# Kernel tuning notes

Measured on AMD Instinct MI355X. Metric: run time of the kernel, lower is better.

The kernel has to match this reference:

```python
import jax, jax.numpy as jnp
import numpy as np

B, G, K, KD = 16384, 17, 12, 16      # batch, games, kicks/game, kick feature dim
DK, DM, H, T = 16, 32, 2, 4          # d_kick, d_model, n_attn_heads, n_targets
SD, H1, H2, HH = 64, 256, 128, 32    # static_dim, backbone hidden dims, head hidden
AO = H * DM                          # attention output dim = 64
EPS = 1e-5
NEG_INF = float('-inf')


def setup_inputs() -> dict:
    ks = jax.random.split(jax.random.key(0), 18)
    n = lambda i, s, sc=0.05: jax.random.normal(ks[i], s, jnp.float32) * sc
    x_static = jax.random.normal(ks[0], (B, SD), jnp.float32)
    x_kicks = jax.random.normal(ks[1], (B, G, K, KD), jnp.float32)
    # masks: True = real game / kick; force position 0 valid so no row is fully padded
    outer_mask = jax.random.bernoulli(ks[2], 0.9, (B, G)).at[:, 0].set(True)
    inner_mask = jax.random.bernoulli(ks[3], 0.85, (B, G, K)).at[:, :, 0].set(True)
    return dict(
        x_static=x_static, x_kicks=x_kicks,
        W_ke=n(4, (KD, DK)), b_ke=jnp.zeros((DK,), jnp.float32),
        q_inner=n(5, (1, DK), 0.02),
        W_ge=n(6, (DK, DM)), b_ge=jnp.zeros((DM,), jnp.float32),
        pos_emb=n(7, (G, DM), 0.02),
        q_outer=n(8, (T * H, DM), 0.02),
        log_temp=jnp.zeros((T,), jnp.float32),
        ln_g=jnp.ones((T, AO), jnp.float32), ln_b=jnp.zeros((T, AO), jnp.float32),
        W1=n(9, (SD, H1)), b1=jnp.zeros((H1,), jnp.float32),
        g1=jnp.ones((H1,), jnp.float32), be1=jnp.zeros((H1,), jnp.float32),
        m1=n(10, (H1,)), v1=jax.random.uniform(ks[11], (H1,), jnp.float32) + 0.5,
        W2=n(12, (H1, H2)), b2=jnp.zeros((H2,), jnp.float32),
        g2=jnp.ones((H2,), jnp.float32), be2=jnp.zeros((H2,), jnp.float32),
        m2=n(13, (H2,)), v2=jax.random.uniform(ks[14], (H2,), jnp.float32) + 0.5,
        Wh1=n(15, (T, H2 + AO, HH)), bh1=jnp.zeros((T, HH), jnp.float32),
        Wh2=n(16, (T, HH)), bh2=jnp.zeros((T,), jnp.float32),
        outer_mask=outer_mask, inner_mask=inner_mask)


def _forward(x_static, x_kicks, W_ke, b_ke, q_inner, W_ge, b_ge, pos_emb,
             q_outer, log_temp, ln_g, ln_b, W1, b1, g1, be1, m1, v1,
             W2, b2, g2, be2, m2, v2, Wh1, bh1, Wh2, bh2,
             outer_mask, inner_mask):
    # kick encoder: Linear -> ReLU, [B,G,K,KD] -> [B,G,K,DK]
    kick_enc = jax.nn.relu(jnp.einsum('bgkd,de->bgke', x_kicks, W_ke) + b_ke)
    # inner AttentionPool: single learned query over kicks within each game
    ai = jnp.einsum('d,bgkd->bgk', q_inner[0], kick_enc) * (DK ** -0.5)
    ai = jnp.where(inner_mask, ai, NEG_INF)
    wi = jnp.nan_to_num(jax.nn.softmax(ai, axis=-1))       # all-masked rows -> 0
    per_game = jnp.einsum('bgk,bgkd->bgd', wi, kick_enc)   # [B,G,DK]
    # game encoder + learned positional embedding
    encoded = jax.nn.relu(per_game @ W_ge + b_ge) + pos_emb[None]  # [B,G,DM]
    # outer AttentionPool: T*H learned queries over games, per-target temperature
    ao = jnp.einsum('qd,bgd->bqg', q_outer, encoded) * (DM ** -0.5)
    ao = ao * jnp.repeat(jnp.exp(-log_temp), H)[None, :, None]
    ao = jnp.where(outer_mask[:, None, :], ao, NEG_INF)
    wo = jnp.nan_to_num(jax.nn.softmax(ao, axis=-1))
    pooled = jnp.einsum('bqg,bgd->bqd', wo, encoded).reshape(-1, T, AO)  # [B,T,64]
    # per-target LayerNorm on history vector
    mu = pooled.mean(-1, keepdims=True)
    var = ((pooled - mu) ** 2).mean(-1, keepdims=True)
    hist = (pooled - mu) * jax.lax.rsqrt(var + EPS) * ln_g[None] + ln_b[None]
    # backbone: Linear -> BatchNorm(eval) -> ReLU, x2 (dropout = identity in eval)
    z = jax.nn.relu((x_static @ W1 + b1 - m1) * jax.lax.rsqrt(v1 + EPS) * g1 + be1)
    z = jax.nn.relu((z @ W2 + b2 - m2) * jax.lax.rsqrt(v2 + EPS) * g2 + be2)
    # per-target heads on [shared_static ; history_vec]
    head_in = jnp.concatenate(
        [jnp.broadcast_to(z[:, None, :], (z.shape[0], T, H2)), hist], axis=-1)  # [B,T,192]
    h = jax.nn.relu(jnp.einsum('btd,tdh->bth', head_in, Wh1) + bh1[None])
    out = jnp.einsum('bth,th->bt', h, Wh2) + bh2[None]
    return jnp.maximum(out, 0.0)  # all targets non-negative (clamp, not softplus)


def reference(x_static, x_kicks, W_ke, b_ke, q_inner, W_ge, b_ge, pos_emb,
              q_outer, log_temp, ln_g, ln_b, W1, b1, g1, be1, m1, v1,
              W2, b2, g2, be2, m2, v2, Wh1, bh1, Wh2, bh2,
              outer_mask, inner_mask):
    return _forward(x_static, x_kicks, W_ke, b_ke, q_inner, W_ge, b_ge, pos_emb,
                    q_outer, log_temp, ln_g, ln_b, W1, b1, g1, be1, m1, v1,
                    W2, b2, g2, be2, m2, v2, Wh1, bh1, Wh2, bh2,
                    outer_mask, inner_mask)
```

## Files before the change

kernel.cpp:

```cpp
#include <hip/hip_runtime.h>
#include <math.h>

#define NEGM (-1e30f)

__device__ __forceinline__ float4 ld4(const float* p) { return *(const float4*)p; }
__device__ __forceinline__ void fma4(float4& a, float s, const float4 w) {
    a.x += s * w.x; a.y += s * w.y; a.z += s * w.z; a.w += s * w.w;
}
__device__ __forceinline__ float dot4(const float4 a, const float4 b) {
    return (a.x * b.x + a.y * b.y) + (a.z * b.z + a.w * b.w);
}
__device__ __forceinline__ void upd4(float4& p, float rm, float rw, const float4 a) {
    p.x = p.x * rm + rw * a.x; p.y = p.y * rm + rw * a.y;
    p.z = p.z * rm + rw * a.z; p.w = p.w * rm + rw * a.w;
}
__device__ __forceinline__ void relu4(float4& a) {
    a.x = fmaxf(a.x, 0.f); a.y = fmaxf(a.y, 0.f);
    a.z = fmaxf(a.z, 0.f); a.w = fmaxf(a.w, 0.f);
}

__global__ __launch_bounds__(256) void hist_kernel(
    const float* __restrict__ x_kicks,
    const float* __restrict__ W_ke, const float* __restrict__ b_ke,
    const float* __restrict__ q_inner,
    const float* __restrict__ W_ge, const float* __restrict__ b_ge,
    const float* __restrict__ pos_emb, const float* __restrict__ q_outer,
    const float* __restrict__ log_temp,
    const float* __restrict__ ln_g, const float* __restrict__ ln_b,
    const int* __restrict__ outer_mask, const int* __restrict__ inner_mask,
    float* __restrict__ hist)
{
    __shared__ float s_wge[512];
    __shared__ float s_qout[256];
    __shared__ float s_part[4][51 * 20];
    __shared__ float s_enc[4][17 * 36];
    __shared__ float s_ao[4][136];

    const int tid  = threadIdx.x;
    const int wid  = tid >> 6;
    const int lane = tid & 63;
    const int b    = blockIdx.x * 4 + wid;

    s_qout[tid] = q_outer[tid];
    s_wge[tid] = W_ge[tid];
    s_wge[tid + 256] = W_ge[tid + 256];
    __syncthreads();

    float* part = s_part[wid];
    float* enc  = s_enc[wid];
    float* ao   = s_ao[wid];

    {
        const int lp = (lane < 51) ? lane : 50;
        const float* xb = x_kicks + ((size_t)b * 204 + lp * 4) * 16;
        const int4 msk = *(const int4*)(inner_mask + (size_t)b * 204 + lp * 4);

        const float4 qi0 = ld4(q_inner + 0), qi1 = ld4(q_inner + 4);
        const float4 qi2 = ld4(q_inner + 8), qi3 = ld4(q_inner + 12);
        const float4 bk0 = ld4(b_ke + 0), bk1 = ld4(b_ke + 4);
        const float4 bk2 = ld4(b_ke + 8), bk3 = ld4(b_ke + 12);

        float m = NEGM, s = 0.f;
        float4 p0 = {0,0,0,0}, p1 = p0, p2 = p0, p3 = p0;

        #pragma unroll
        for (int pp = 0; pp < 4; ++pp) {
            float xs[16];
            {
                float4 x0 = ld4(xb + pp * 16 + 0), x1 = ld4(xb + pp * 16 + 4);
                float4 x2 = ld4(xb + pp * 16 + 8), x3 = ld4(xb + pp * 16 + 12);
                xs[0]=x0.x; xs[1]=x0.y; xs[2]=x0.z; xs[3]=x0.w;
                xs[4]=x1.x; xs[5]=x1.y; xs[6]=x1.z; xs[7]=x1.w;
                xs[8]=x2.x; xs[9]=x2.y; xs[10]=x2.z; xs[11]=x2.w;
                xs[12]=x3.x; xs[13]=x3.y; xs[14]=x3.z; xs[15]=x3.w;
            }
            float4 a0 = bk0, a1 = bk1, a2 = bk2, a3 = bk3;
            #pragma unroll
            for (int i = 0; i < 16; ++i) {
                float xi = xs[i];
                fma4(a0, xi, ld4(W_ke + i * 16 + 0));
                fma4(a1, xi, ld4(W_ke + i * 16 + 4));
                fma4(a2, xi, ld4(W_ke + i * 16 + 8));
                fma4(a3, xi, ld4(W_ke + i * 16 + 12));
            }
            relu4(a0); relu4(a1); relu4(a2); relu4(a3);

            float sc = (dot4(a0, qi0) + dot4(a1, qi1) + dot4(a2, qi2) + dot4(a3, qi3)) * 0.25f;
            int mk = (pp == 0) ? msk.x : (pp == 1) ? msk.y : (pp == 2) ? msk.z : msk.w;

            float scm = mk ? sc : NEGM;
            float mn = fmaxf(m, scm);
            float rm = __expf(m - mn);
            float rw = mk ? __expf(sc - mn) : 0.f;
            s = s * rm + rw;
            upd4(p0, rm, rw, a0); upd4(p1, rm, rw, a1);
            upd4(p2, rm, rw, a2); upd4(p3, rm, rw, a3);
            m = mn;
        }

        const int base = (lp / 3) * 3;
        float gm = fmaxf(fmaxf(__shfl(m, base), __shfl(m, base + 1)), __shfl(m, base + 2));
        float r  = __expf(m - gm);
        float sl = s * r;
        float gs = __shfl(sl, base) + __shfl(sl, base + 1) + __shfl(sl, base + 2);
        float c  = r / gs;
        p0.x*=c; p0.y*=c; p0.z*=c; p0.w*=c;
        p1.x*=c; p1.y*=c; p1.z*=c; p1.w*=c;
        p2.x*=c; p2.y*=c; p2.z*=c; p2.w*=c;
        p3.x*=c; p3.y*=c; p3.z*=c; p3.w*=c;
        if (lane < 51) {
            *(float4*)&part[lane * 20 + 0]  = p0;
            *(float4*)&part[lane * 20 + 4]  = p1;
            *(float4*)&part[lane * 20 + 8]  = p2;
            *(float4*)&part[lane * 20 + 12] = p3;
        }
    }
    __syncthreads();

    for (int t = lane; t < 136; t += 64) {
        const int g = t >> 3, dq = t & 7;
        const float* pp0 = &part[(3 * g) * 20];
        float4 acc = ld4(b_ge + dq * 4);
        #pragma unroll
        for (int i4 = 0; i4 < 4; ++i4) {
            float4 qa = *(float4*)(pp0 + i4 * 4);
            float4 qb = *(float4*)(pp0 + 20 + i4 * 4);
            float4 qc = *(float4*)(pp0 + 40 + i4 * 4);
            float4 pg4;
            pg4.x = qa.x + qb.x + qc.x; pg4.y = qa.y + qb.y + qc.y;
            pg4.z = qa.z + qb.z + qc.z; pg4.w = qa.w + qb.w + qc.w;
            fma4(acc, pg4.x, *(float4*)&s_wge[(i4 * 4 + 0) * 32 + dq * 4]);
            fma4(acc, pg4.y, *(float4*)&s_wge[(i4 * 4 + 1) * 32 + dq * 4]);
            fma4(acc, pg4.z, *(float4*)&s_wge[(i4 * 4 + 2) * 32 + dq * 4]);
            fma4(acc, pg4.w, *(float4*)&s_wge[(i4 * 4 + 3) * 32 + dq * 4]);
        }
        float4 pe = ld4(pos_emb + g * 32 + dq * 4);
        acc.x = fmaxf(acc.x, 0.f) + pe.x; acc.y = fmaxf(acc.y, 0.f) + pe.y;
        acc.z = fmaxf(acc.z, 0.f) + pe.z; acc.w = fmaxf(acc.w, 0.f) + pe.w;
        *(float4*)&enc[g * 36 + dq * 4] = acc;
    }
    __syncthreads();

    for (int t = lane; t < 136; t += 64) {
        const int q = t / 17, g = t - q * 17;
        float4 acc = {0.f, 0.f, 0.f, 0.f};
        #pragma unroll
        for (int i4 = 0; i4 < 8; ++i4) {
            float4 ev = *(float4*)&enc[g * 36 + i4 * 4];
            float4 qv = *(float4*)&s_qout[q * 32 + i4 * 4];
            acc.x += ev.x * qv.x; acc.y += ev.y * qv.y;
            acc.z += ev.z * qv.z; acc.w += ev.w * qv.w;
        }
        float sv = (acc.x + acc.y) + (acc.z + acc.w);
        sv *= 0.17677669529663687f * __expf(-log_temp[q >> 1]);
        ao[t] = outer_mask[b * 17 + g] ? sv : NEGM;
    }
    __syncthreads();

    {
        const int q = lane >> 3, j = lane & 7;
        float s0 = ao[q * 17 + j];
        float s1 = ao[q * 17 + j + 8];
        float s2 = (j == 0) ? ao[q * 17 + 16] : NEGM;
        float mx = fmaxf(fmaxf(s0, s1), s2);
        mx = fmaxf(mx, __shfl_xor(mx, 1));
        mx = fmaxf(mx, __shfl_xor(mx, 2));
        mx = fmaxf(mx, __shfl_xor(mx, 4));
        float e0 = __expf(s0 - mx), e1 = __expf(s1 - mx);
        float e2 = (j == 0) ? __expf(s2 - mx) : 0.f;
        float ssum = e0 + e1 + e2;
        ssum += __shfl_xor(ssum, 1);
        ssum += __shfl_xor(ssum, 2);
        ssum += __shfl_xor(ssum, 4);
        float inv = 1.f / ssum;
        ao[q * 17 + j] = e0 * inv;
        ao[q * 17 + j + 8] = e1 * inv;
        if (j == 0) ao[q * 17 + 16] = e2 * inv;
    }
    __syncthreads();

    {
        const int q = lane >> 3, dq = lane & 7;
        float4 acc = {0.f, 0.f, 0.f, 0.f};
        #pragma unroll
        for (int g = 0; g < 17; ++g) {
            float w = ao[q * 17 + g];
            fma4(acc, w, *(float4*)&enc[g * 36 + dq * 4]);
        }
        float sv = (acc.x + acc.y) + (acc.z + acc.w);
        sv += __shfl_xor(sv, 1); sv += __shfl_xor(sv, 2);
        sv += __shfl_xor(sv, 4); sv += __shfl_xor(sv, 8);
        float mu = sv * 0.015625f;
        float4 d;
        d.x = acc.x - mu; d.y = acc.y - mu; d.z = acc.z - mu; d.w = acc.w - mu;
        float v = (d.x * d.x + d.y * d.y) + (d.z * d.z + d.w * d.w);
        v += __shfl_xor(v, 1); v += __shfl_xor(v, 2);
        v += __shfl_xor(v, 4); v += __shfl_xor(v, 8);
        float rs = rsqrtf(v * 0.015625f + 1e-5f);
        float4 gam = ld4(ln_g + lane * 4);
        float4 bet = ld4(ln_b + lane * 4);
        float4 res;
        res.x = d.x * rs * gam.x + bet.x; res.y = d.y * rs * gam.y + bet.y;
        res.z = d.z * rs * gam.z + bet.z; res.w = d.w * rs * gam.w + bet.w;
        *(float4*)&hist[(size_t)b * 256 + lane * 4] = res;
    }
}

__global__ __launch_bounds__(256) void backbone_kernel(
    const float* __restrict__ x_static,
    const float* __restrict__ W1, const float* __restrict__ b1,
    const float* __restrict__ g1, const float* __restrict__ be1,
    const float* __restrict__ m1, const float* __restrict__ v1,
    const float* __restrict__ W2, const float* __restrict__ b2,
    const float* __restrict__ g2, const float* __restrict__ be2,
    const float* __restrict__ m2, const float* __restrict__ v2,
    const float* __restrict__ Wh1, const float* __restrict__ bh1,
    const float* __restrict__ Wh2, const float* __restrict__ bh2,
    const float* __restrict__ hist, float* __restrict__ out)
{
    __shared__ float s_x[16 * 64];
    __shared__ float s_z1[16 * 256];
    __shared__ float s_z2[16 * 132];

    const int tid = threadIdx.x;
    const int row0 = blockIdx.x * 16;

    *(float4*)&s_x[tid * 4] = ld4(x_static + (size_t)row0 * 64 + tid * 4);
    __syncthreads();

    {
        const int col = tid;
        float acc[16];
        #pragma unroll
        for (int r = 0; r < 16; ++r) acc[r] = 0.f;
        for (int k4 = 0; k4 < 16; ++k4) {
            float w0 = W1[(k4 * 4 + 0) * 256 + col];
            float w1 = W1[(k4 * 4 + 1) * 256 + col];
            float w2 = W1[(k4 * 4 + 2) * 256 + col];
            float w3 = W1[(k4 * 4 + 3) * 256 + col];
            #pragma unroll
            for (int r = 0; r < 16; ++r) {
                float4 xv = *(float4*)&s_x[r * 64 + k4 * 4];
                acc[r] += xv.x * w0 + xv.y * w1 + xv.z * w2 + xv.w * w3;
            }
        }
        float sc = rsqrtf(v1[col] + 1e-5f) * g1[col];
        float off = b1[col] - m1[col];
        float bb = be1[col];
        #pragma unroll
        for (int r = 0; r < 16; ++r)
            s_z1[r * 256 + col] = fmaxf((acc[r] + off) * sc + bb, 0.f);
    }
    __syncthreads();

    {
        const int col = tid & 127;
        const int r0 = (tid >> 7) * 8;
        float acc[8];
        #pragma unroll
        for (int r = 0; r < 8; ++r) acc[r] = 0.f;
        for (int k4 = 0; k4 < 64; ++k4) {
            float w0 = W2[(k4 * 4 + 0) * 128 + col];
            float w1 = W2[(k4 * 4 + 1) * 128 + col];
            float w2 = W2[(k4 * 4 + 2) * 128 + col];
            float w3 = W2[(k4 * 4 + 3) * 128 + col];
            #pragma unroll
            for (int r = 0; r < 8; ++r) {
                float4 zv = *(float4*)&s_z1[(r0 + r) * 256 + k4 * 4];
                acc[r] += zv.x * w0 + zv.y * w1 + zv.z * w2 + zv.w * w3;
            }
        }
        float sc = rsqrtf(v2[col] + 1e-5f) * g2[col];
        float off = b2[col] - m2[col];
        float bb = be2[col];
        #pragma unroll
        for (int r = 0; r < 8; ++r)
            s_z2[(r0 + r) * 132 + col] = fmaxf((acc[r] + off) * sc + bb, 0.f);
    }
    __syncthreads();

    {
        const int p = tid >> 2;
        const int gl = tid & 3;
        const int row = p >> 2;
        const int tgt = p & 3;
        const int j0 = gl * 8;

        float acc[8];
        #pragma unroll
        for (int j = 0; j < 8; ++j) acc[j] = bh1[tgt * 32 + j0 + j];

        const float* w1p = Wh1 + (size_t)tgt * 192 * 32 + j0;
        for (int d4 = 0; d4 < 32; ++d4) {
            float4 zv = *(float4*)&s_z2[row * 132 + d4 * 4];
            #pragma unroll
            for (int c = 0; c < 4; ++c) {
                float v = (c == 0) ? zv.x : (c == 1) ? zv.y : (c == 2) ? zv.z : zv.w;
                float4 a = ld4(w1p + (d4 * 4 + c) * 32);
                float4 bq = ld4(w1p + (d4 * 4 + c) * 32 + 4);
                acc[0] += v * a.x;  acc[1] += v * a.y;  acc[2] += v * a.z;  acc[3] += v * a.w;
                acc[4] += v * bq.x; acc[5] += v * bq.y; acc[6] += v * bq.z; acc[7] += v * bq.w;
            }
        }
        const float* hp = hist + (size_t)(row0 + row) * 256 + tgt * 64;
        const float* w1q = w1p + 128 * 32;
        for (int d4 = 0; d4 < 16; ++d4) {
            float4 hv = ld4(hp + d4 * 4);
            #pragma unroll
            for (int c = 0; c < 4; ++c) {
                float v = (c == 0) ? hv.x : (c == 1) ? hv.y : (c == 2) ? hv.z : hv.w;
                float4 a = ld4(w1q + (d4 * 4 + c) * 32);
                float4 bq = ld4(w1q + (d4 * 4 + c) * 32 + 4);
                acc[0] += v * a.x;  acc[1] += v * a.y;  acc[2] += v * a.z;  acc[3] += v * a.w;
                acc[4] += v * bq.x; acc[5] += v * bq.y; acc[6] += v * bq.z; acc[7] += v * bq.w;
            }
        }
        float ps = 0.f;
        #pragma unroll
        for (int j = 0; j < 8; ++j) ps += fmaxf(acc[j], 0.f) * Wh2[tgt * 32 + j0 + j];
        ps += __shfl_xor(ps, 1);
        ps += __shfl_xor(ps, 2);
        if (gl == 0) out[(size_t)(row0 + row) * 4 + tgt] = fmaxf(ps + bh2[tgt], 0.f);
    }
}

extern "C" void kernel_launch(void* const* d_in, const int* in_sizes, int n_in,
                              void* d_out, int out_size, void* d_ws, size_t ws_size,
                              hipStream_t stream) {
    const float* x_static = (const float*)d_in[0];
    const float* x_kicks  = (const float*)d_in[1];
    const float* W_ke     = (const float*)d_in[2];
    const float* b_ke     = (const float*)d_in[3];
    const float* q_inner  = (const float*)d_in[4];
    const float* W_ge     = (const float*)d_in[5];
    const float* b_ge     = (const float*)d_in[6];
    const float* pos_emb  = (const float*)d_in[7];
    const float* q_outer  = (const float*)d_in[8];
    const float* log_temp = (const float*)d_in[9];
    const float* ln_g     = (const float*)d_in[10];
    const float* ln_b     = (const float*)d_in[11];
    const float* W1       = (const float*)d_in[12];
    const float* b1       = (const float*)d_in[13];
    const float* g1       = (const float*)d_in[14];
    const float* be1      = (const float*)d_in[15];
    const float* m1       = (const float*)d_in[16];
    const float* v1       = (const float*)d_in[17];
    const float* W2       = (const float*)d_in[18];
    const float* b2       = (const float*)d_in[19];
    const float* g2       = (const float*)d_in[20];
    const float* be2      = (const float*)d_in[21];
    const float* m2       = (const float*)d_in[22];
    const float* v2       = (const float*)d_in[23];
    const float* Wh1      = (const float*)d_in[24];
    const float* bh1      = (const float*)d_in[25];
    const float* Wh2      = (const float*)d_in[26];
    const float* bh2      = (const float*)d_in[27];
    const int* outer_mask = (const int*)d_in[28];
    const int* inner_mask = (const int*)d_in[29];

    float* hist = (float*)d_ws;
    float* out  = (float*)d_out;

    hist_kernel<<<16384 / 4, 256, 0, stream>>>(
        x_kicks, W_ke, b_ke, q_inner, W_ge, b_ge, pos_emb, q_outer,
        log_temp, ln_g, ln_b, outer_mask, inner_mask, hist);

    backbone_kernel<<<16384 / 16, 256, 0, stream>>>(
        x_static, W1, b1, g1, be1, m1, v1, W2, b2, g2, be2, m2, v2,
        Wh1, bh1, Wh2, bh2, hist, out);
}
```

Before: 153.9 us.

## Use packed float2 FMA math and reorganize backbone GEMM thread mapping

Converts the kick encoder, backbone matmuls and head matmul to two-wide float vector types so the compiler can emit packed FP32 FMA instructions. W_ke is staged in shared memory. The per-game three-lane partial sums are now reduced with shuffles instead of through shared memory, which shrinks the shared buffer. The backbone layers are remapped so each thread computes two adjacent columns over fewer rows, which lowers redundant shared loads. This adds more shuffles and changes register pressure and the global weight access pattern.

```diff
diff --git a/kernel.cpp b/kernel.cpp
--- a/kernel.cpp
+++ b/kernel.cpp
@@ -2,21 +2,15 @@
 #include <math.h>
 
 #define NEGM (-1e30f)
+
+typedef float v2f __attribute__((ext_vector_type(2)));
 
 __device__ __forceinline__ float4 ld4(const float* p) { return *(const float4*)p; }
 __device__ __forceinline__ void fma4(float4& a, float s, const float4 w) {
     a.x += s * w.x; a.y += s * w.y; a.z += s * w.z; a.w += s * w.w;
 }
-__device__ __forceinline__ float dot4(const float4 a, const float4 b) {
-    return (a.x * b.x + a.y * b.y) + (a.z * b.z + a.w * b.w);
-}
-__device__ __forceinline__ void upd4(float4& p, float rm, float rw, const float4 a) {
-    p.x = p.x * rm + rw * a.x; p.y = p.y * rm + rw * a.y;
-    p.z = p.z * rm + rw * a.z; p.w = p.w * rm + rw * a.w;
-}
-__device__ __forceinline__ void relu4(float4& a) {
-    a.x = fmaxf(a.x, 0.f); a.y = fmaxf(a.y, 0.f);
-    a.z = fmaxf(a.z, 0.f); a.w = fmaxf(a.w, 0.f);
+__device__ __forceinline__ v2f max0v(v2f a) {
+    a.x = fmaxf(a.x, 0.f); a.y = fmaxf(a.y, 0.f); return a;
 }
 
 __global__ __launch_bounds__(256) void hist_kernel(
@@ -30,9 +24,10 @@
     const int* __restrict__ outer_mask, const int* __restrict__ inner_mask,
     float* __restrict__ hist)
 {
+    __shared__ float s_wke[256];
     __shared__ float s_wge[512];
     __shared__ float s_qout[256];
-    __shared__ float s_part[4][51 * 20];
+    __shared__ float s_pg[4][17 * 20];
     __shared__ float s_enc[4][17 * 36];
     __shared__ float s_ao[4][136];
 
@@ -41,27 +36,31 @@
     const int lane = tid & 63;
     const int b    = blockIdx.x * 4 + wid;
 
+    s_wke[tid] = W_ke[tid];
     s_qout[tid] = q_outer[tid];
     s_wge[tid] = W_ge[tid];
     s_wge[tid + 256] = W_ge[tid + 256];
     __syncthreads();
 
-    float* part = s_part[wid];
-    float* enc  = s_enc[wid];
-    float* ao   = s_ao[wid];
-
-    {
-        const int lp = (lane < 51) ? lane : 50;
-        const float* xb = x_kicks + ((size_t)b * 204 + lp * 4) * 16;
-        const int4 msk = *(const int4*)(inner_mask + (size_t)b * 204 + lp * 4);
-
-        const float4 qi0 = ld4(q_inner + 0), qi1 = ld4(q_inner + 4);
-        const float4 qi2 = ld4(q_inner + 8), qi3 = ld4(q_inner + 12);
-        const float4 bk0 = ld4(b_ke + 0), bk1 = ld4(b_ke + 4);
-        const float4 bk2 = ld4(b_ke + 8), bk3 = ld4(b_ke + 12);
+    float* pg  = s_pg[wid];
+    float* enc = s_enc[wid];
+    float* ao  = s_ao[wid];
+
+    if (lane < 51) {
+        const float* xb = x_kicks + ((size_t)b * 204 + lane * 4) * 16;
+        const int4 msk = *(const int4*)(inner_mask + (size_t)b * 204 + lane * 4);
+
+        v2f qv[8], bk[8];
+        #pragma unroll
+        for (int j = 0; j < 8; ++j) {
+            qv[j] = *(const v2f*)(q_inner + 2 * j);
+            bk[j] = *(const v2f*)(b_ke + 2 * j);
+        }
 
         float m = NEGM, s = 0.f;
-        float4 p0 = {0,0,0,0}, p1 = p0, p2 = p0, p3 = p0;
+        v2f p[8];
+        #pragma unroll
+        for (int j = 0; j < 8; ++j) p[j] = v2f{0.f, 0.f};
 
         #pragma unroll
         for (int pp = 0; pp < 4; ++pp) {
@@ -74,18 +73,23 @@
                 xs[8]=x2.x; xs[9]=x2.y; xs[10]=x2.z; xs[11]=x2.w;
                 xs[12]=x3.x; xs[13]=x3.y; xs[14]=x3.z; xs[15]=x3.w;
             }
-            float4 a0 = bk0, a1 = bk1, a2 = bk2, a3 = bk3;
+            v2f a[8];
+            #pragma unroll
+            for (int j = 0; j < 8; ++j) a[j] = bk[j];
             #pragma unroll
             for (int i = 0; i < 16; ++i) {
-                float xi = xs[i];
-                fma4(a0, xi, ld4(W_ke + i * 16 + 0));
-                fma4(a1, xi, ld4(W_ke + i * 16 + 4));
-                fma4(a2, xi, ld4(W_ke + i * 16 + 8));
-                fma4(a3, xi, ld4(W_ke + i * 16 + 12));
-            }
-            relu4(a0); relu4(a1); relu4(a2); relu4(a3);
-
-            float sc = (dot4(a0, qi0) + dot4(a1, qi1) + dot4(a2, qi2) + dot4(a3, qi3)) * 0.25f;
+                v2f xi = {xs[i], xs[i]};
+                const v2f* wrow = (const v2f*)&s_wke[i * 16];
+                #pragma unroll
+                for (int j = 0; j < 8; ++j) a[j] += xi * wrow[j];
+            }
+            #pragma unroll
+            for (int j = 0; j < 8; ++j) a[j] = max0v(a[j]);
+
+            v2f dv = {0.f, 0.f};
+            #pragma unroll
+            for (int j = 0; j < 8; ++j) dv += a[j] * qv[j];
+            float sc = (dv.x + dv.y) * 0.25f;
             int mk = (pp == 0) ? msk.x : (pp == 1) ? msk.y : (pp == 2) ? msk.z : msk.w;
 
             float scm = mk ? sc : NEGM;
@@ -93,46 +97,45 @@
             float rm = __expf(m - mn);
             float rw = mk ? __expf(sc - mn) : 0.f;
             s = s * rm + rw;
-            upd4(p0, rm, rw, a0); upd4(p1, rm, rw, a1);
-            upd4(p2, rm, rw, a2); upd4(p3, rm, rw, a3);
+            v2f rmv = {rm, rm}, rwv = {rw, rw};
+            #pragma unroll
+            for (int j = 0; j < 8; ++j) p[j] = p[j] * rmv + a[j] * rwv;
             m = mn;
         }
 
-        const int base = (lp / 3) * 3;
+        const int base = (lane / 3) * 3;
         float gm = fmaxf(fmaxf(__shfl(m, base), __shfl(m, base + 1)), __shfl(m, base + 2));
         float r  = __expf(m - gm);
         float sl = s * r;
         float gs = __shfl(sl, base) + __shfl(sl, base + 1) + __shfl(sl, base + 2);
         float c  = r / gs;
-        p0.x*=c; p0.y*=c; p0.z*=c; p0.w*=c;
-        p1.x*=c; p1.y*=c; p1.z*=c; p1.w*=c;
-        p2.x*=c; p2.y*=c; p2.z*=c; p2.w*=c;
-        p3.x*=c; p3.y*=c; p3.z*=c; p3.w*=c;
-        if (lane < 51) {
-            *(float4*)&part[lane * 20 + 0]  = p0;
-            *(float4*)&part[lane * 20 + 4]  = p1;
-            *(float4*)&part[lane * 20 + 8]  = p2;
-            *(float4*)&part[lane * 20 + 12] = p3;
+        v2f cv = {c, c};
+        #pragma unroll
+        for (int j = 0; j < 8; ++j) p[j] *= cv;
+
+        float o[16];
+        #pragma unroll
+        for (int j = 0; j < 8; ++j) {
+            o[2*j]   = __shfl(p[j].x, base) + __shfl(p[j].x, base + 1) + __shfl(p[j].x, base + 2);
+            o[2*j+1] = __shfl(p[j].y, base) + __shfl(p[j].y, base + 1) + __shfl(p[j].y, base + 2);
+        }
+        if (lane == base) {
+            const int g = lane / 3;
+            *(float4*)&pg[g * 20 + 0]  = make_float4(o[0],  o[1],  o[2],  o[3]);
+            *(float4*)&pg[g * 20 + 4]  = make_float4(o[4],  o[5],  o[6],  o[7]);
+            *(float4*)&pg[g * 20 + 8]  = make_float4(o[8],  o[9],  o[10], o[11]);
+            *(float4*)&pg[g * 20 + 12] = make_float4(o[12], o[13], o[14], o[15]);
         }
     }
     __syncthreads();
 
     for (int t = lane; t < 136; t += 64) {
         const int g = t >> 3, dq = t & 7;
-        const float* pp0 = &part[(3 * g) * 20];
         float4 acc = ld4(b_ge + dq * 4);
         #pragma unroll
-        for (int i4 = 0; i4 < 4; ++i4) {
-            float4 qa = *(float4*)(pp0 + i4 * 4);
-            float4 qb = *(float4*)(pp0 + 20 + i4 * 4);
-            float4 qc = *(float4*)(pp0 + 40 + i4 * 4);
-            float4 pg4;
-            pg4.x = qa.x + qb.x + qc.x; pg4.y = qa.y + qb.y + qc.y;
-            pg4.z = qa.z + qb.z + qc.z; pg4.w = qa.w + qb.w + qc.w;
-            fma4(acc, pg4.x, *(float4*)&s_wge[(i4 * 4 + 0) * 32 + dq * 4]);
-            fma4(acc, pg4.y, *(float4*)&s_wge[(i4 * 4 + 1) * 32 + dq * 4]);
-            fma4(acc, pg4.z, *(float4*)&s_wge[(i4 * 4 + 2) * 32 + dq * 4]);
-            fma4(acc, pg4.w, *(float4*)&s_wge[(i4 * 4 + 3) * 32 + dq * 4]);
+        for (int i = 0; i < 16; ++i) {
+            float pv = pg[g * 20 + i];
+            fma4(acc, pv, *(float4*)&s_wge[i * 32 + dq * 4]);
         }
         float4 pe = ld4(pos_emb + g * 32 + dq * 4);
         acc.x = fmaxf(acc.x, 0.f) + pe.x; acc.y = fmaxf(acc.y, 0.f) + pe.y;
@@ -147,9 +150,9 @@
         #pragma unroll
         for (int i4 = 0; i4 < 8; ++i4) {
             float4 ev = *(float4*)&enc[g * 36 + i4 * 4];
-            float4 qv = *(float4*)&s_qout[q * 32 + i4 * 4];
-            acc.x += ev.x * qv.x; acc.y += ev.y * qv.y;
-            acc.z += ev.z * qv.z; acc.w += ev.w * qv.w;
+            float4 qvv = *(float4*)&s_qout[q * 32 + i4 * 4];
+            acc.x += ev.x * qvv.x; acc.y += ev.y * qvv.y;
+            acc.z += ev.z * qvv.z; acc.w += ev.w * qvv.w;
         }
         float sv = (acc.x + acc.y) + (acc.z + acc.w);
         sv *= 0.17677669529663687f * __expf(-log_temp[q >> 1]);
@@ -229,53 +232,70 @@
     __syncthreads();
 
     {
-        const int col = tid;
-        float acc[16];
-        #pragma unroll
-        for (int r = 0; r < 16; ++r) acc[r] = 0.f;
+        const int cp = tid & 127;
+        const int r0 = (tid >> 7) * 8;
+        v2f acc[8];
+        #pragma unroll
+        for (int r = 0; r < 8; ++r) acc[r] = v2f{0.f, 0.f};
         for (int k4 = 0; k4 < 16; ++k4) {
-            float w0 = W1[(k4 * 4 + 0) * 256 + col];
-            float w1 = W1[(k4 * 4 + 1) * 256 + col];
-            float w2 = W1[(k4 * 4 + 2) * 256 + col];
-            float w3 = W1[(k4 * 4 + 3) * 256 + col];
-            #pragma unroll
-            for (int r = 0; r < 16; ++r) {
-                float4 xv = *(float4*)&s_x[r * 64 + k4 * 4];
-                acc[r] += xv.x * w0 + xv.y * w1 + xv.z * w2 + xv.w * w3;
-            }
-        }
-        float sc = rsqrtf(v1[col] + 1e-5f) * g1[col];
-        float off = b1[col] - m1[col];
-        float bb = be1[col];
-        #pragma unroll
-        for (int r = 0; r < 16; ++r)
-            s_z1[r * 256 + col] = fmaxf((acc[r] + off) * sc + bb, 0.f);
-    }
-    __syncthreads();
-
-    {
-        const int col = tid & 127;
-        const int r0 = (tid >> 7) * 8;
-        float acc[8];
-        #pragma unroll
-        for (int r = 0; r < 8; ++r) acc[r] = 0.f;
+            float4 xv[8];
+            #pragma unroll
+            for (int r = 0; r < 8; ++r) xv[r] = *(float4*)&s_x[(r0 + r) * 64 + k4 * 4];
+            #pragma unroll
+            for (int c = 0; c < 4; ++c) {
+                v2f w2 = *(const v2f*)&W1[(k4 * 4 + c) * 256 + 2 * cp];
+                #pragma unroll
+                for (int r = 0; r < 8; ++r) {
+                    float xc = (c == 0) ? xv[r].x : (c == 1) ? xv[r].y : (c == 2) ? xv[r].z : xv[r].w;
+                    v2f xb = {xc, xc};
+                    acc[r] += xb * w2;
+                }
+            }
+        }
+        v2f v1v = *(const v2f*)(v1 + 2 * cp);
+        v2f g1v = *(const v2f*)(g1 + 2 * cp);
+        v2f b1v = *(const v2f*)(b1 + 2 * cp);
+        v2f m1v = *(const v2f*)(m1 + 2 * cp);
+        v2f e1v = *(const v2f*)(be1 + 2 * cp);
+        v2f scv; scv.x = rsqrtf(v1v.x + 1e-5f) * g1v.x; scv.y = rsqrtf(v1v.y + 1e-5f) * g1v.y;
+        v2f offv = b1v - m1v;
+        #pragma unroll
+        for (int r = 0; r < 8; ++r)
+            *(v2f*)&s_z1[(r0 + r) * 256 + 2 * cp] = max0v((acc[r] + offv) * scv + e1v);
+    }
+    __syncthreads();
+
+    {
+        const int cp = tid & 63;
+        const int q = tid >> 6;
+        v2f acc[4];
+        #pragma unroll
+        for (int r = 0; r < 4; ++r) acc[r] = v2f{0.f, 0.f};
         for (int k4 = 0; k4 < 64; ++k4) {
-            float w0 = W2[(k4 * 4 + 0) * 128 + col];
-            float w1 = W2[(k4 * 4 + 1) * 128 + col];
-            float w2 = W2[(k4 * 4 + 2) * 128 + col];
-            float w3 = W2[(k4 * 4 + 3) * 128 + col];
-            #pragma unroll
-            for (int r = 0; r < 8; ++r) {
-                float4 zv = *(float4*)&s_z1[(r0 + r) * 256 + k4 * 4];
-                acc[r] += zv.x * w0 + zv.y * w1 + zv.z * w2 + zv.w * w3;
-            }
-        }
-        float sc = rsqrtf(v2[col] + 1e-5f) * g2[col];
-        float off = b2[col] - m2[col];
-        float bb = be2[col];
-        #pragma unroll
-        for (int r = 0; r < 8; ++r)
-            s_z2[(r0 + r) * 132 + col] = fmaxf((acc[r] + off) * sc + bb, 0.f);
+            float4 zv[4];
+            #pragma unroll
+            for (int r = 0; r < 4; ++r) zv[r] = *(float4*)&s_z1[(4 * q + r) * 256 + k4 * 4];
+            #pragma unroll
+            for (int c = 0; c < 4; ++c) {
+                v2f w2 = *(const v2f*)&W2[(k4 * 4 + c) * 128 + 2 * cp];
+                #pragma unroll
+                for (int r = 0; r < 4; ++r) {
+                    float zc = (c == 0) ? zv[r].x : (c == 1) ? zv[r].y : (c == 2) ? zv[r].z : zv[r].w;
+                    v2f zb = {zc, zc};
+                    acc[r] += zb * w2;
+                }
+            }
+        }
+        v2f v2v = *(const v2f*)(v2 + 2 * cp);
+        v2f g2v = *(const v2f*)(g2 + 2 * cp);
+        v2f b2v = *(const v2f*)(b2 + 2 * cp);
+        v2f m2v = *(const v2f*)(m2 + 2 * cp);
+        v2f e2v = *(const v2f*)(be2 + 2 * cp);
+        v2f scv; scv.x = rsqrtf(v2v.x + 1e-5f) * g2v.x; scv.y = rsqrtf(v2v.y + 1e-5f) * g2v.y;
+        v2f offv = b2v - m2v;
+        #pragma unroll
+        for (int r = 0; r < 4; ++r)
+            *(v2f*)&s_z2[(4 * q + r) * 132 + 2 * cp] = max0v((acc[r] + offv) * scv + e2v);
     }
     __syncthreads();
 
@@ -286,9 +306,9 @@
         const int tgt = p & 3;
         const int j0 = gl * 8;
 
-        float acc[8];
-        #pragma unroll
-        for (int j = 0; j < 8; ++j) acc[j] = bh1[tgt * 32 + j0 + j];
+        v2f acc[4];
+        #pragma unroll
+        for (int j = 0; j < 4; ++j) acc[j] = *(const v2f*)(bh1 + tgt * 32 + j0 + 2 * j);
 
         const float* w1p = Wh1 + (size_t)tgt * 192 * 32 + j0;
         for (int d4 = 0; d4 < 32; ++d4) {
@@ -296,10 +316,10 @@
             #pragma unroll
             for (int c = 0; c < 4; ++c) {
                 float v = (c == 0) ? zv.x : (c == 1) ? zv.y : (c == 2) ? zv.z : zv.w;
-                float4 a = ld4(w1p + (d4 * 4 + c) * 32);
-                float4 bq = ld4(w1p + (d4 * 4 + c) * 32 + 4);
-                acc[0] += v * a.x;  acc[1] += v * a.y;  acc[2] += v * a.z;  acc[3] += v * a.w;
-                acc[4] += v * bq.x; acc[5] += v * bq.y; acc[6] += v * bq.z; acc[7] += v * bq.w;
+                v2f vb = {v, v};
+                const v2f* wp = (const v2f*)(w1p + (d4 * 4 + c) * 32);
+                #pragma unroll
+                for (int j = 0; j < 4; ++j) acc[j] += vb * wp[j];
             }
         }
         const float* hp = hist + (size_t)(row0 + row) * 256 + tgt * 64;
@@ -309,15 +329,18 @@
             #pragma unroll
             for (int c = 0; c < 4; ++c) {
                 float v = (c == 0) ? hv.x : (c == 1) ? hv.y : (c == 2) ? hv.z : hv.w;
-                float4 a = ld4(w1q + (d4 * 4 + c) * 32);
-                float4 bq = ld4(w1q + (d4 * 4 + c) * 32 + 4);
-                acc[0] += v * a.x;  acc[1] += v * a.y;  acc[2] += v * a.z;  acc[3] += v * a.w;
-                acc[4] += v * bq.x; acc[5] += v * bq.y; acc[6] += v * bq.z; acc[7] += v * bq.w;
+                v2f vb = {v, v};
+                const v2f* wp = (const v2f*)(w1q + (d4 * 4 + c) * 32);
+                #pragma unroll
+                for (int j = 0; j < 4; ++j) acc[j] += vb * wp[j];
             }
         }
         float ps = 0.f;
         #pragma unroll
-        for (int j = 0; j < 8; ++j) ps += fmaxf(acc[j], 0.f) * Wh2[tgt * 32 + j0 + j];
+        for (int j = 0; j < 4; ++j) {
+            ps += fmaxf(acc[j].x, 0.f) * Wh2[tgt * 32 + j0 + 2 * j];
+            ps += fmaxf(acc[j].y, 0.f) * Wh2[tgt * 32 + j0 + 2 * j + 1];
+        }
         ps += __shfl_xor(ps, 1);
         ps += __shfl_xor(ps, 2);
         if (gl == 0) out[(size_t)(row0 + row) * 4 + tgt] = fmaxf(ps + bh2[tgt], 0.f);
```

After: 161.2 us. +4.7%, slower.

## Stage W_ke in LDS, reduce game partials via shuffles, halve hist block size

Applied to the files above, without the earlier changes.

Moves the kick-encoder weight matrix into shared memory so the inner FMA loop reads LDS instead of global/constant loads. The three per-lane partial pooled vectors for each game are now summed with wavefront shuffles and written once per game, which shrinks the shared partial buffer and simplifies the W_ge projection loop. The hist kernel now runs 2 waves (128 threads) per block instead of 4, which lowers LDS use per block and allows more blocks per CU. The costs are extra shuffle instructions and more, smaller blocks.

```diff
diff --git a/kernel.cpp b/kernel.cpp
--- a/kernel.cpp
+++ b/kernel.cpp
@@ -14,12 +14,8 @@
     p.x = p.x * rm + rw * a.x; p.y = p.y * rm + rw * a.y;
     p.z = p.z * rm + rw * a.z; p.w = p.w * rm + rw * a.w;
 }
-__device__ __forceinline__ void relu4(float4& a) {
-    a.x = fmaxf(a.x, 0.f); a.y = fmaxf(a.y, 0.f);
-    a.z = fmaxf(a.z, 0.f); a.w = fmaxf(a.w, 0.f);
-}
-
-__global__ __launch_bounds__(256) void hist_kernel(
+
+__global__ __launch_bounds__(128) void hist_kernel(
     const float* __restrict__ x_kicks,
     const float* __restrict__ W_ke, const float* __restrict__ b_ke,
     const float* __restrict__ q_inner,
@@ -30,30 +26,35 @@
     const int* __restrict__ outer_mask, const int* __restrict__ inner_mask,
     float* __restrict__ hist)
 {
+    __shared__ float s_wke[256];
     __shared__ float s_wge[512];
     __shared__ float s_qout[256];
-    __shared__ float s_part[4][51 * 20];
-    __shared__ float s_enc[4][17 * 36];
-    __shared__ float s_ao[4][136];
+    __shared__ float s_pg[2][17 * 20];
+    __shared__ float s_enc[2][17 * 36];
+    __shared__ float s_ao[2][136];
 
     const int tid  = threadIdx.x;
     const int wid  = tid >> 6;
     const int lane = tid & 63;
-    const int b    = blockIdx.x * 4 + wid;
-
+    const int b    = blockIdx.x * 2 + wid;
+
+    s_wke[tid] = W_ke[tid];
+    s_wke[tid + 128] = W_ke[tid + 128];
     s_qout[tid] = q_outer[tid];
+    s_qout[tid + 128] = q_outer[tid + 128];
     s_wge[tid] = W_ge[tid];
+    s_wge[tid + 128] = W_ge[tid + 128];
     s_wge[tid + 256] = W_ge[tid + 256];
-    __syncthreads();
-
-    float* part = s_part[wid];
-    float* enc  = s_enc[wid];
-    float* ao   = s_ao[wid];
-
-    {
-        const int lp = (lane < 51) ? lane : 50;
-        const float* xb = x_kicks + ((size_t)b * 204 + lp * 4) * 16;
-        const int4 msk = *(const int4*)(inner_mask + (size_t)b * 204 + lp * 4);
+    s_wge[tid + 384] = W_ge[tid + 384];
+    __syncthreads();
+
+    float* pg  = s_pg[wid];
+    float* enc = s_enc[wid];
+    float* ao  = s_ao[wid];
+
+    if (lane < 51) {
+        const float* xb = x_kicks + ((size_t)b * 204 + lane * 4) * 16;
+        const int4 msk = *(const int4*)(inner_mask + (size_t)b * 204 + lane * 4);
 
         const float4 qi0 = ld4(q_inner + 0), qi1 = ld4(q_inner + 4);
         const float4 qi2 = ld4(q_inner + 8), qi3 = ld4(q_inner + 12);
@@ -78,12 +79,15 @@
             #pragma unroll
             for (int i = 0; i < 16; ++i) {
                 float xi = xs[i];
-                fma4(a0, xi, ld4(W_ke + i * 16 + 0));
-                fma4(a1, xi, ld4(W_ke + i * 16 + 4));
-                fma4(a2, xi, ld4(W_ke + i * 16 + 8));
-                fma4(a3, xi, ld4(W_ke + i * 16 + 12));
-            }
-            relu4(a0); relu4(a1); relu4(a2); relu4(a3);
+                fma4(a0, xi, *(float4*)&s_wke[i * 16 + 0]);
+                fma4(a1, xi, *(float4*)&s_wke[i * 16 + 4]);
+                fma4(a2, xi, *(float4*)&s_wke[i * 16 + 8]);
+                fma4(a3, xi, *(float4*)&s_wke[i * 16 + 12]);
+            }
+            a0.x=fmaxf(a0.x,0.f); a0.y=fmaxf(a0.y,0.f); a0.z=fmaxf(a0.z,0.f); a0.w=fmaxf(a0.w,0.f);
+            a1.x=fmaxf(a1.x,0.f); a1.y=fmaxf(a1.y,0.f); a1.z=fmaxf(a1.z,0.f); a1.w=fmaxf(a1.w,0.f);
+            a2.x=fmaxf(a2.x,0.f); a2.y=fmaxf(a2.y,0.f); a2.z=fmaxf(a2.z,0.f); a2.w=fmaxf(a2.w,0.f);
+            a3.x=fmaxf(a3.x,0.f); a3.y=fmaxf(a3.y,0.f); a3.z=fmaxf(a3.z,0.f); a3.w=fmaxf(a3.w,0.f);
 
             float sc = (dot4(a0, qi0) + dot4(a1, qi1) + dot4(a2, qi2) + dot4(a3, qi3)) * 0.25f;
             int mk = (pp == 0) ? msk.x : (pp == 1) ? msk.y : (pp == 2) ? msk.z : msk.w;
@@ -98,7 +102,7 @@
             m = mn;
         }
 
-        const int base = (lp / 3) * 3;
+        const int base = (lane / 3) * 3;
         float gm = fmaxf(fmaxf(__shfl(m, base), __shfl(m, base + 1)), __shfl(m, base + 2));
         float r  = __expf(m - gm);
         float sl = s * r;
@@ -108,31 +112,41 @@
         p1.x*=c; p1.y*=c; p1.z*=c; p1.w*=c;
         p2.x*=c; p2.y*=c; p2.z*=c; p2.w*=c;
         p3.x*=c; p3.y*=c; p3.z*=c; p3.w*=c;
-        if (lane < 51) {
-            *(float4*)&part[lane * 20 + 0]  = p0;
-            *(float4*)&part[lane * 20 + 4]  = p1;
-            *(float4*)&part[lane * 20 + 8]  = p2;
-            *(float4*)&part[lane * 20 + 12] = p3;
+
+        float4 o0, o1, o2, o3;
+        o0.x = __shfl(p0.x,base)+__shfl(p0.x,base+1)+__shfl(p0.x,base+2);
+        o0.y = __shfl(p0.y,base)+__shfl(p0.y,base+1)+__shfl(p0.y,base+2);
+        o0.z = __shfl(p0.z,base)+__shfl(p0.z,base+1)+__shfl(p0.z,base+2);
+        o0.w = __shfl(p0.w,base)+__shfl(p0.w,base+1)+__shfl(p0.w,base+2);
+        o1.x = __shfl(p1.x,base)+__shfl(p1.x,base+1)+__shfl(p1.x,base+2);
+        o1.y = __shfl(p1.y,base)+__shfl(p1.y,base+1)+__shfl(p1.y,base+2);
+        o1.z = __shfl(p1.z,base)+__shfl(p1.z,base+1)+__shfl(p1.z,base+2);
+        o1.w = __shfl(p1.w,base)+__shfl(p1.w,base+1)+__shfl(p1.w,base+2);
+        o2.x = __shfl(p2.x,base)+__shfl(p2.x,base+1)+__shfl(p2.x,base+2);
+        o2.y = __shfl(p2.y,base)+__shfl(p2.y,base+1)+__shfl(p2.y,base+2);
+        o2.z = __shfl(p2.z,base)+__shfl(p2.z,base+1)+__shfl(p2.z,base+2);
+        o2.w = __shfl(p2.w,base)+__shfl(p2.w,base+1)+__shfl(p2.w,base+2);
+        o3.x = __shfl(p3.x,base)+__shfl(p3.x,base+1)+__shfl(p3.x,base+2);
+        o3.y = __shfl(p3.y,base)+__shfl(p3.y,base+1)+__shfl(p3.y,base+2);
+        o3.z = __shfl(p3.z,base)+__shfl(p3.z,base+1)+__shfl(p3.z,base+2);
+        o3.w = __shfl(p3.w,base)+__shfl(p3.w,base+1)+__shfl(p3.w,base+2);
+        if (lane == base) {
+            const int g = lane / 3;
+            *(float4*)&pg[g * 20 + 0]  = o0;
+            *(float4*)&pg[g * 20 + 4]  = o1;
+            *(float4*)&pg[g * 20 + 8]  = o2;
+            *(float4*)&pg[g * 20 + 12] = o3;
         }
     }
     __syncthreads();
 
     for (int t = lane; t < 136; t += 64) {
         const int g = t >> 3, dq = t & 7;
-        const float* pp0 = &part[(3 * g) * 20];
         float4 acc = ld4(b_ge + dq * 4);
         #pragma unroll
-        for (int i4 = 0; i4 < 4; ++i4) {
-            float4 qa = *(float4*)(pp0 + i4 * 4);
-            float4 qb = *(float4*)(pp0 + 20 + i4 * 4);
-            float4 qc = *(float4*)(pp0 + 40 + i4 * 4);
-            float4 pg4;
-            pg4.x = qa.x + qb.x + qc.x; pg4.y = qa.y + qb.y + qc.y;
-            pg4.z = qa.z + qb.z + qc.z; pg4.w = qa.w + qb.w + qc.w;
-            fma4(acc, pg4.x, *(float4*)&s_wge[(i4 * 4 + 0) * 32 + dq * 4]);
-            fma4(acc, pg4.y, *(float4*)&s_wge[(i4 * 4 + 1) * 32 + dq * 4]);
-            fma4(acc, pg4.z, *(float4*)&s_wge[(i4 * 4 + 2) * 32 + dq * 4]);
-            fma4(acc, pg4.w, *(float4*)&s_wge[(i4 * 4 + 3) * 32 + dq * 4]);
+        for (int i = 0; i < 16; ++i) {
+            float pv = pg[g * 20 + i];
+            fma4(acc, pv, *(float4*)&s_wge[i * 32 + dq * 4]);
         }
         float4 pe = ld4(pos_emb + g * 32 + dq * 4);
         acc.x = fmaxf(acc.x, 0.f) + pe.x; acc.y = fmaxf(acc.y, 0.f) + pe.y;
@@ -361,7 +375,7 @@
     float* hist = (float*)d_ws;
     float* out  = (float*)d_out;
 
-    hist_kernel<<<16384 / 4, 256, 0, stream>>>(
+    hist_kernel<<<16384 / 2, 128, 0, stream>>>(
         x_kicks, W_ke, b_ke, q_inner, W_ge, b_ge, pos_emb, q_outer,
         log_temp, ln_g, ln_b, outer_mask, inner_mask, hist);
 
```

After: 148.3 us. -3.7%, faster.
